# Performance work log

Measured on AMD Instinct MI355X. Metric: run time of the kernel, lower is better.

The kernel has to match this reference:

```python
import jax, jax.numpy as jnp
import numpy as np

HIDDEN = 2048
HEADS = 16
HEAD_DIM = HIDDEN // HEADS          # 128
KV_RANK = HIDDEN // 8               # 256 (kv_compression_ratio = 8)
ATTN_DIM = HEADS * HEAD_DIM         # 2048
EPS = 1e-6


def setup_inputs() -> dict:
    key = jax.random.key(0)
    ks = jax.random.split(key, 6)
    B, L = 2, 2048
    x = jax.random.normal(ks[0], (B, L, HIDDEN), dtype=jnp.float32)
    # weights stored [in, out] (torch Linear applies x @ W.T; same math)
    s = lambda fan_in: 1.0 / np.sqrt(fan_in)
    Wq = jax.random.normal(ks[1], (HIDDEN, ATTN_DIM), dtype=jnp.float32) * s(HIDDEN)
    Wkv_down = jax.random.normal(ks[2], (HIDDEN, KV_RANK), dtype=jnp.float32) * s(HIDDEN)
    kv_norm_w = jnp.ones((KV_RANK,), dtype=jnp.float32)
    Wkv_up = jax.random.normal(ks[3], (KV_RANK, 2 * ATTN_DIM), dtype=jnp.float32) * s(KV_RANK)
    Wo = jax.random.normal(ks[4], (ATTN_DIM, HIDDEN), dtype=jnp.float32) * s(ATTN_DIM)
    return {"x": x, "Wq": Wq, "Wkv_down": Wkv_down, "kv_norm_w": kv_norm_w,
            "Wkv_up": Wkv_up, "Wo": Wo}


def rms_norm(x, w):
    ms = jnp.mean(x * x, axis=-1, keepdims=True)
    return w * (x * jax.lax.rsqrt(ms + EPS))


def reference(x, Wq, Wkv_down, kv_norm_w, Wkv_up, Wo):
    B, L, D = x.shape
    q = (x @ Wq).reshape(B, L, HEADS, HEAD_DIM)
    latent = rms_norm(x @ Wkv_down, kv_norm_w)            # [B, L, KV_RANK]
    kv = latent @ Wkv_up                                   # [B, L, 2*ATTN_DIM]
    k, v = jnp.split(kv, 2, axis=-1)
    k = k.reshape(B, L, HEADS, HEAD_DIM)
    v = v.reshape(B, L, HEADS, HEAD_DIM)
    scores = jnp.einsum('bxhd,byhd->bhxy', q, k) / np.sqrt(HEAD_DIM)
    causal = jnp.tril(jnp.ones((L, L), dtype=bool))
    scores = jnp.where(causal, scores, -jnp.inf)
    attn = jax.nn.softmax(scores, axis=-1)
    out = jnp.einsum('bhxy,byhd->bxhd', attn, v).reshape(B, L, ATTN_DIM)
    return out @ Wo
```

## Files before the change

kernel.cpp:

```cpp
#include <hip/hip_runtime.h>
#include <cstdint>
#include <cstddef>

typedef unsigned short u16;
typedef __bf16 bf16x8 __attribute__((ext_vector_type(8)));
typedef __bf16 bf16x2 __attribute__((ext_vector_type(2)));
typedef float f32x4 __attribute__((ext_vector_type(4)));

__device__ inline u16 f2bf(float f) {
  uint32_t u = __builtin_bit_cast(uint32_t, f);
  u += 0x7fffu + ((u >> 16) & 1u);
  return (u16)(u >> 16);
}

#if defined(__has_builtin)
#if __has_builtin(__builtin_amdgcn_cvt_pk_bf16_f32)
#define HAVE_PK_BF16 1
#endif
#endif

__device__ inline uint32_t pk2bf(float a, float b) {
#ifdef HAVE_PK_BF16
  bf16x2 v = __builtin_amdgcn_cvt_pk_bf16_f32(a, b);
  return __builtin_bit_cast(uint32_t, v);
#else
  return (uint32_t)f2bf(a) | ((uint32_t)f2bf(b) << 16);
#endif
}

__device__ inline f32x4 mfma16(bf16x8 a, bf16x8 b, f32x4 c) {
  return __builtin_amdgcn_mfma_f32_16x16x32_bf16(a, b, c, 0, 0, 0);
}

__device__ inline void gl_lds16(const u16* g, u16* l) {
  __builtin_amdgcn_global_load_lds(
      (const __attribute__((address_space(1))) uint32_t*)g,
      (__attribute__((address_space(3))) uint32_t*)l, 16, 0, 0);
}

__device__ void tcvt_dev(const float* __restrict__ in, u16* __restrict__ out,
                         int R, int C, int bx, int by, float (*t)[33], int tid) {
  int cb = bx * 32, rb = by * 32;
  int x = tid & 31, y = tid >> 5;
#pragma unroll
  for (int k = 0; k < 4; ++k)
    t[y + k * 8][x] = in[(size_t)(rb + y + k * 8) * C + cb + x];
  __syncthreads();
#pragma unroll
  for (int k = 0; k < 4; ++k)
    out[(size_t)(cb + y + k * 8) * R + rb + x] = f2bf(t[x][y + k * 8]);
}

__global__ __launch_bounds__(256) void k_prep(
    const float* __restrict__ x, const float* __restrict__ Wq,
    const float* __restrict__ Wkvd, const float* __restrict__ Wkvu,
    const float* __restrict__ Wo, u16* __restrict__ xbf,
    u16* __restrict__ WqkdT, u16* __restrict__ WkvuT, u16* __restrict__ WoT) {
  __shared__ float t[32][33];
  int bid = blockIdx.x, tid = threadIdx.x;
  if (bid < 8192) {
    int i = bid * 256 + tid;
    const float4 v = ((const float4*)x)[i];
    ushort4 o;
    o.x = f2bf(v.x); o.y = f2bf(v.y); o.z = f2bf(v.z); o.w = f2bf(v.w);
    ((ushort4*)xbf)[i] = o;
  } else if (bid < 12288) {
    int q = bid - 8192;
    tcvt_dev(Wq, WqkdT, 2048, 2048, q & 63, q >> 6, t, tid);
  } else if (bid < 12800) {
    int q = bid - 12288;
    tcvt_dev(Wkvd, WqkdT + 2048 * 2048, 2048, 256, q & 7, q >> 3, t, tid);
  } else if (bid < 13824) {
    int q = bid - 12800;
    tcvt_dev(Wkvu, WkvuT, 256, 4096, q & 127, q >> 7, t, tid);
  } else {
    int q = bid - 13824;
    tcvt_dev(Wo, WoT, 2048, 2048, q & 63, q >> 6, t, tid);
  }
}

__global__ __launch_bounds__(256) void k_rmsn(const u16* __restrict__ qc,
                                              const float* __restrict__ w,
                                              u16* __restrict__ out) {
  int row = blockIdx.x * 4 + (threadIdx.x >> 6);
  int lane = threadIdx.x & 63;
  const ushort4 u = *(const ushort4*)(qc + (size_t)row * 2304 + 2048 + lane * 4);
  float4 v;
  v.x = __builtin_bit_cast(float, (uint32_t)u.x << 16);
  v.y = __builtin_bit_cast(float, (uint32_t)u.y << 16);
  v.z = __builtin_bit_cast(float, (uint32_t)u.z << 16);
  v.w = __builtin_bit_cast(float, (uint32_t)u.w << 16);
  float ss = v.x * v.x + v.y * v.y + v.z * v.z + v.w * v.w;
#pragma unroll
  for (int off = 1; off < 64; off <<= 1) ss += __shfl_xor(ss, off);
  float r = rsqrtf(ss * (1.f / 256.f) + 1e-6f);
  const float4 wv = ((const float4*)w)[lane];
  ushort4 o;
  o.x = f2bf(v.x * r * wv.x);
  o.y = f2bf(v.y * r * wv.y);
  o.z = f2bf(v.z * r * wv.z);
  o.w = f2bf(v.w * r * wv.w);
  *(ushort4*)(out + (size_t)row * 256 + lane * 4) = o;
}

template <int BK, int MODE>
__global__ __launch_bounds__(256) void k_gemm(const u16* __restrict__ A,
                                              const u16* __restrict__ BT,
                                              void* __restrict__ C,
                                              u16* __restrict__ C2, int K,
                                              int ldc, float scale) {
  __shared__ __align__(16) u16 As[128 * BK];
  __shared__ __align__(16) u16 Bs[128 * BK];
  const int tid = threadIdx.x, wave = tid >> 6, lane = tid & 63;
  const int lanem = lane & 15, quad = lane >> 4;
  const int m0 = blockIdx.x * 128, n0 = blockIdx.y * 128;
  const int wr = wave >> 1, wc = wave & 1;
  f32x4 acc[4][4] = {};
  for (int k0 = 0; k0 < K; k0 += BK) {
    __syncthreads();
    if constexpr (BK == 32) {
      const int srow = lane >> 2, scol = (lane & 3) * 8;
#pragma unroll
      for (int c = 0; c < 2; ++c) {
        int p = wave * 2 + c;
        gl_lds16(A + (size_t)(m0 + p * 16 + srow) * K + k0 + scol, &As[p * 512]);
        gl_lds16(BT + (size_t)(n0 + p * 16 + srow) * K + k0 + scol, &Bs[p * 512]);
      }
    } else {
      const int srow = lane >> 3;
      const int scol = ((lane & 7) ^ srow) * 8;
#pragma unroll
      for (int c = 0; c < 4; ++c) {
        int p = wave * 4 + c;
        gl_lds16(A + (size_t)(m0 + p * 8 + srow) * K + k0 + scol, &As[p * 512]);
        gl_lds16(BT + (size_t)(n0 + p * 8 + srow) * K + k0 + scol, &Bs[p * 512]);
      }
    }
    __syncthreads();
#pragma unroll
    for (int kk = 0; kk < BK / 32; ++kk) {
      bf16x8 af[4], bff[4];
      if constexpr (BK == 32) {
#pragma unroll
        for (int i = 0; i < 4; ++i)
          af[i] = *(const bf16x8*)&As[(wr * 64 + i * 16 + lanem) * 32 + quad * 8];
#pragma unroll
        for (int j = 0; j < 4; ++j)
          bff[j] = *(const bf16x8*)&Bs[(wc * 64 + j * 16 + lanem) * 32 + quad * 8];
      } else {
        const int kp = ((kk * 4 + quad) ^ (lanem & 7)) << 3;
#pragma unroll
        for (int i = 0; i < 4; ++i)
          af[i] = *(const bf16x8*)&As[(wr * 64 + i * 16 + lanem) * 64 + kp];
#pragma unroll
        for (int j = 0; j < 4; ++j)
          bff[j] = *(const bf16x8*)&Bs[(wc * 64 + j * 16 + lanem) * 64 + kp];
      }
#pragma unroll
      for (int i = 0; i < 4; ++i)
#pragma unroll
        for (int j = 0; j < 4; ++j)
          acc[i][j] = mfma16(af[i], bff[j], acc[i][j]);
    }
  }
#pragma unroll
  for (int i = 0; i < 4; ++i)
#pragma unroll
    for (int j = 0; j < 4; ++j)
#pragma unroll
      for (int r = 0; r < 4; ++r) {
        int row = m0 + wr * 64 + i * 16 + quad * 4 + r;
        int col = n0 + wc * 64 + j * 16 + lanem;
        float v = acc[i][j][r] * scale;
        if constexpr (MODE == 0) {
          ((float*)C)[(size_t)row * ldc + col] = v;
        } else if constexpr (MODE == 1) {
          ((u16*)C)[(size_t)row * ldc + col] = f2bf(v);
        } else {
          if (n0 < 2048) {
            ((u16*)C)[(size_t)row * 2048 + col] = f2bf(v);
          } else {
            int cc = col - 2048, hh = cc >> 7, dd = cc & 127;
            int bb = row >> 11, ll = row & 2047;
            C2[((size_t)(bb * 16 + hh) * 128 + dd) * 2048 + ll] = f2bf(v);
          }
        }
      }
}

__global__ __launch_bounds__(256) void k_attn(const u16* __restrict__ qg,
                                              const u16* __restrict__ kg,
                                              const u16* __restrict__ vtg,
                                              u16* __restrict__ ao) {
  __shared__ __align__(16) u16 Ks[2][64 * 128];
  __shared__ __align__(16) u16 VTs[2][128 * 64];
  __shared__ __align__(16) u16 Ps[4][16 * 72];
  const int bid = blockIdx.x;
  const int xcd = bid & 7, r5 = bid >> 3;
  const int bh = xcd * 4 + (r5 & 3), pairid = r5 >> 2;
  const int b = bh >> 4, h = bh & 15;
  const int tid = threadIdx.x, w = tid >> 6, lane = tid & 63;
  const int lanem = lane & 15, quad = lane >> 4;

  const int kr = lane >> 4, kc = lane & 15;
  const u16* kbp[4];
#pragma unroll
  for (int j = 0; j < 4; ++j) {
    int row = w * 16 + j * 4 + kr;
    kbp[j] = kg + (size_t)(b * 2048 + row) * 2048 + h * 128 +
             ((kc ^ (row & 15)) << 3);
  }
  const int vr = lane >> 3, vc = lane & 7;
  const u16* vbp[4];
#pragma unroll
  for (int j = 0; j < 4; ++j) {
    int row = w * 32 + j * 8 + vr;
    vbp[j] = vtg + (size_t)(bh * 128 + row) * 2048 + ((vc ^ vr) << 3);
  }

  const int qt0 = pairid, qt1 = 31 - pairid;
  int qb = qt0 * 64, nt = qt0 + 1, t = 0, qi = 0;

  bf16x8 qf[4];
  {
    const u16* qp = qg + (size_t)(b * 2048 + qb + w * 16 + lanem) * 2304 +
                    h * 128 + quad * 8;
#pragma unroll
    for (int c = 0; c < 4; ++c) qf[c] = *(const bf16x8*)(qp + c * 32);
  }
  f32x4 o[8] = {};
  float m_i = -1e30f, l_i = 0.f;

#pragma unroll
  for (int j = 0; j < 4; ++j) gl_lds16(kbp[j], &Ks[0][(w * 16 + j * 4) * 128]);
#pragma unroll
  for (int j = 0; j < 4; ++j) gl_lds16(vbp[j], &VTs[0][(w * 32 + j * 8) * 64]);

  for (int it = 0; it < 33; ++it) {
    __syncthreads();
    if (it + 1 < 33) {
      int t2 = (t + 1 == nt) ? 0 : t + 1;
      int nb = (it + 1) & 1;
      size_t ko = (size_t)t2 * (64 * 2048);
      int vo = t2 * 64;
#pragma unroll
      for (int j = 0; j < 4; ++j)
        gl_lds16(kbp[j] + ko, &Ks[nb][(w * 16 + j * 4) * 128]);
#pragma unroll
      for (int j = 0; j < 4; ++j)
        gl_lds16(vbp[j] + vo, &VTs[nb][(w * 32 + j * 8) * 64]);
    }
    const int buf = it & 1;
    f32x4 s[4] = {};
#pragma unroll
    for (int c = 0; c < 4; ++c) {
      const int kp = ((c * 4 + quad) ^ lanem) << 3;
#pragma unroll
      for (int ss = 0; ss < 4; ++ss) {
        bf16x8 kf = *(const bf16x8*)&Ks[buf][(ss * 16 + lanem) * 128 + kp];
        s[ss] = mfma16(kf, qf[c], s[ss]);
      }
    }
    if (t == nt - 1) {
      const int qq = w * 16 + lanem;
#pragma unroll
      for (int ss = 0; ss < 4; ++ss)
#pragma unroll
        for (int r = 0; r < 4; ++r)
          if (ss * 16 + quad * 4 + r > qq) s[ss][r] = -1e30f;
    }
    float mx = fmaxf(fmaxf(fmaxf(s[0][0], s[0][1]), fmaxf(s[0][2], s[0][3])),
                     fmaxf(fmaxf(s[1][0], s[1][1]), fmaxf(s[1][2], s[1][3])));
    mx = fmaxf(mx, fmaxf(fmaxf(fmaxf(s[2][0], s[2][1]), fmaxf(s[2][2], s[2][3])),
                         fmaxf(fmaxf(s[3][0], s[3][1]), fmaxf(s[3][2], s[3][3]))));
    mx = fmaxf(mx, __shfl_xor(mx, 16));
    mx = fmaxf(mx, __shfl_xor(mx, 32));
    const float mn = fmaxf(m_i, mx);
    float rs = 0.f;
#pragma unroll
    for (int ss = 0; ss < 4; ++ss)
#pragma unroll
      for (int r = 0; r < 4; ++r) {
        s[ss][r] = exp2f(s[ss][r] - mn);
        rs += s[ss][r];
      }
    rs += __shfl_xor(rs, 16);
    rs += __shfl_xor(rs, 32);
    if (__any(mx > m_i)) {
      const float al = exp2f(m_i - mn);
      l_i = l_i * al + rs;
      m_i = mn;
      float alr[4];
#pragma unroll
      for (int r = 0; r < 4; ++r)
        alr[r] = __shfl(al, (lane & 48) | (quad * 4 + r));
#pragma unroll
      for (int dc = 0; dc < 8; ++dc)
#pragma unroll
        for (int r = 0; r < 4; ++r) o[dc][r] *= alr[r];
    } else {
      l_i += rs;
    }
#pragma unroll
    for (int ss = 0; ss < 4; ++ss) {
      uint2 pp;
      pp.x = pk2bf(s[ss][0], s[ss][1]);
      pp.y = pk2bf(s[ss][2], s[ss][3]);
      *(uint2*)&Ps[w][lanem * 72 + ss * 16 + quad * 4] = pp;
    }
    bf16x8 pf0 = *(const bf16x8*)&Ps[w][lanem * 72 + quad * 8];
    bf16x8 pf1 = *(const bf16x8*)&Ps[w][lanem * 72 + 32 + quad * 8];
#pragma unroll
    for (int dc = 0; dc < 8; ++dc) {
      const int vrow = (dc * 16 + lanem) * 64;
      bf16x8 vf0 = *(const bf16x8*)&VTs[buf][vrow + ((quad ^ (lanem & 7)) << 3)];
      bf16x8 vf1 =
          *(const bf16x8*)&VTs[buf][vrow + (((4 + quad) ^ (lanem & 7)) << 3)];
      o[dc] = mfma16(pf0, vf0, o[dc]);
      o[dc] = mfma16(pf1, vf1, o[dc]);
    }
    if (++t == nt) {
      const float inv = 1.f / l_i;
      float invr[4];
#pragma unroll
      for (int r = 0; r < 4; ++r)
        invr[r] = __shfl(inv, (lane & 48) | (quad * 4 + r));
#pragma unroll
      for (int r = 0; r < 4; ++r) {
        u16* op = ao + (size_t)(b * 2048 + qb + w * 16 + quad * 4 + r) * 2048 +
                  h * 128;
#pragma unroll
        for (int dc = 0; dc < 8; ++dc)
          op[dc * 16 + lanem] = f2bf(o[dc][r] * invr[r]);
      }
      if (qi == 0) {
        qi = 1;
        qb = qt1 * 64;
        nt = qt1 + 1;
        t = 0;
        const u16* qp = qg + (size_t)(b * 2048 + qb + w * 16 + lanem) * 2304 +
                        h * 128 + quad * 8;
#pragma unroll
        for (int c = 0; c < 4; ++c) qf[c] = *(const bf16x8*)(qp + c * 32);
#pragma unroll
        for (int dc = 0; dc < 8; ++dc) o[dc] = f32x4{0.f, 0.f, 0.f, 0.f};
        m_i = -1e30f;
        l_i = 0.f;
      }
    }
  }
}

extern "C" void kernel_launch(void* const* d_in, const int* in_sizes, int n_in,
                              void* d_out, int out_size, void* d_ws, size_t ws_size,
                              hipStream_t stream) {
  const float* x    = (const float*)d_in[0];
  const float* Wq   = (const float*)d_in[1];
  const float* Wkvd = (const float*)d_in[2];
  const float* wn   = (const float*)d_in[3];
  const float* Wkvu = (const float*)d_in[4];
  const float* Wo   = (const float*)d_in[5];
  float* out = (float*)d_out;

  char* w0 = (char*)d_ws;
  u16* xbf   = (u16*)(w0);
  u16* qc    = (u16*)(w0 + 16777216);
  u16* WqkdT = (u16*)(w0 + 35651584);
  u16* WoT   = (u16*)(w0 + 45088768);
  u16* WkvuT = (u16*)(w0 + 53477376);
  u16* kbf   = (u16*)(w0 + 55574528);
  u16* vtbf  = (u16*)(w0 + 72351744);
  u16* latbf = WqkdT;
  u16* aobf  = xbf;

  const float sc2 = 0.08838834764831845f * 1.4426950408889634f;

  k_prep<<<17920, 256, 0, stream>>>(x, Wq, Wkvd, Wkvu, Wo, xbf, WqkdT, WkvuT, WoT);
  k_gemm<32, 1><<<dim3(32, 18), 256, 0, stream>>>(xbf, WqkdT, qc, nullptr, 2048,
                                                  2304, sc2);
  k_rmsn<<<1024, 256, 0, stream>>>(qc, wn, latbf);
  k_gemm<64, 2><<<dim3(32, 32), 256, 0, stream>>>(latbf, WkvuT, kbf, vtbf, 256,
                                                  0, 1.0f);
  k_attn<<<512, 256, 0, stream>>>(qc, kbf, vtbf, aobf);
  k_gemm<32, 0><<<dim3(32, 16), 256, 0, stream>>>(aobf, WoT, out, nullptr, 2048,
                                                  2048, 1.0f);
}
```

Measured before the change: 340.5 us.

## Transpose QK^T layout, compute softmax row sum via ones-column MFMA

The QK^T MFMA operands are swapped so each lane holds four query rows, and row max reductions now use DPP moves instead of cross-lane shuffles. The softmax denominator is computed by appending a block of ones to the V^T tile in LDS and running a ninth MFMA column block, which removes the scalar row-sum and the shuffle-based rescale broadcasts. The P tile in LDS is stored with an XOR swizzle and no padding. Separately, the KV-up GEMM epilogue writes transposed V as packed 4-element stores instead of scalar stores. In exchange it adds extra MFMAs, per-element bf16 stores into P, and more LDS for V^T.

```diff
diff --git a/kernel.cpp b/kernel.cpp
--- a/kernel.cpp
+++ b/kernel.cpp
@@ -13,21 +13,6 @@
   return (u16)(u >> 16);
 }
 
-#if defined(__has_builtin)
-#if __has_builtin(__builtin_amdgcn_cvt_pk_bf16_f32)
-#define HAVE_PK_BF16 1
-#endif
-#endif
-
-__device__ inline uint32_t pk2bf(float a, float b) {
-#ifdef HAVE_PK_BF16
-  bf16x2 v = __builtin_amdgcn_cvt_pk_bf16_f32(a, b);
-  return __builtin_bit_cast(uint32_t, v);
-#else
-  return (uint32_t)f2bf(a) | ((uint32_t)f2bf(b) << 16);
-#endif
-}
-
 __device__ inline f32x4 mfma16(bf16x8 a, bf16x8 b, f32x4 c) {
   return __builtin_amdgcn_mfma_f32_16x16x32_bf16(a, b, c, 0, 0, 0);
 }
@@ -36,6 +21,13 @@
   __builtin_amdgcn_global_load_lds(
       (const __attribute__((address_space(1))) uint32_t*)g,
       (__attribute__((address_space(3))) uint32_t*)l, 16, 0, 0);
+}
+
+template <int CTRL>
+__device__ inline float dppmax(float x) {
+  int y = __builtin_amdgcn_mov_dpp(__builtin_bit_cast(int, x), CTRL, 0xf, 0xf,
+                                   true);
+  return fmaxf(x, __builtin_bit_cast(float, y));
 }
 
 __device__ void tcvt_dev(const float* __restrict__ in, u16* __restrict__ out,
@@ -166,26 +158,33 @@
 #pragma unroll
   for (int i = 0; i < 4; ++i)
 #pragma unroll
-    for (int j = 0; j < 4; ++j)
+    for (int j = 0; j < 4; ++j) {
+      const int row0 = m0 + wr * 64 + i * 16 + quad * 4;
+      const int col = n0 + wc * 64 + j * 16 + lanem;
+      if constexpr (MODE == 2) {
+        if (col >= 2048) {
+          int cc = col - 2048, hh = cc >> 7, dd = cc & 127;
+          int bb = row0 >> 11, ll = row0 & 2047;
+          ushort4 pk;
+          pk.x = f2bf(acc[i][j][0]);
+          pk.y = f2bf(acc[i][j][1]);
+          pk.z = f2bf(acc[i][j][2]);
+          pk.w = f2bf(acc[i][j][3]);
+          *(ushort4*)&C2[((size_t)(bb * 16 + hh) * 128 + dd) * 2048 + ll] = pk;
+          continue;
+        }
+      }
 #pragma unroll
       for (int r = 0; r < 4; ++r) {
-        int row = m0 + wr * 64 + i * 16 + quad * 4 + r;
-        int col = n0 + wc * 64 + j * 16 + lanem;
         float v = acc[i][j][r] * scale;
-        if constexpr (MODE == 0) {
-          ((float*)C)[(size_t)row * ldc + col] = v;
-        } else if constexpr (MODE == 1) {
-          ((u16*)C)[(size_t)row * ldc + col] = f2bf(v);
-        } else {
-          if (n0 < 2048) {
-            ((u16*)C)[(size_t)row * 2048 + col] = f2bf(v);
-          } else {
-            int cc = col - 2048, hh = cc >> 7, dd = cc & 127;
-            int bb = row >> 11, ll = row & 2047;
-            C2[((size_t)(bb * 16 + hh) * 128 + dd) * 2048 + ll] = f2bf(v);
-          }
-        }
-      }
+        if constexpr (MODE == 0)
+          ((float*)C)[(size_t)(row0 + r) * ldc + col] = v;
+        else if constexpr (MODE == 1)
+          ((u16*)C)[(size_t)(row0 + r) * ldc + col] = f2bf(v);
+        else
+          ((u16*)C)[(size_t)(row0 + r) * 2048 + col] = f2bf(v);
+      }
+    }
 }
 
 __global__ __launch_bounds__(256) void k_attn(const u16* __restrict__ qg,
@@ -193,8 +192,8 @@
                                               const u16* __restrict__ vtg,
                                               u16* __restrict__ ao) {
   __shared__ __align__(16) u16 Ks[2][64 * 128];
-  __shared__ __align__(16) u16 VTs[2][128 * 64];
-  __shared__ __align__(16) u16 Ps[4][16 * 72];
+  __shared__ __align__(16) u16 VTs[2][144 * 64];
+  __shared__ __align__(16) u16 Ps[4][16 * 64];
   const int bid = blockIdx.x;
   const int xcd = bid & 7, r5 = bid >> 3;
   const int bh = xcd * 4 + (r5 & 3), pairid = r5 >> 2;
@@ -228,13 +227,20 @@
 #pragma unroll
     for (int c = 0; c < 4; ++c) qf[c] = *(const bf16x8*)(qp + c * 32);
   }
-  f32x4 o[8] = {};
-  float m_i = -1e30f, l_i = 0.f;
+  f32x4 o[9] = {};
+  float m_i[4] = {-1e30f, -1e30f, -1e30f, -1e30f};
 
 #pragma unroll
   for (int j = 0; j < 4; ++j) gl_lds16(kbp[j], &Ks[0][(w * 16 + j * 4) * 128]);
 #pragma unroll
   for (int j = 0; j < 4; ++j) gl_lds16(vbp[j], &VTs[0][(w * 32 + j * 8) * 64]);
+  {
+    const ushort4 ones4{0x3f80u, 0x3f80u, 0x3f80u, 0x3f80u};
+    for (int i = tid; i < 512; i += 256) {
+      int bufi = i >> 8, off = (i & 255) * 4;
+      *(ushort4*)&VTs[bufi][128 * 64 + off] = ones4;
+    }
+  }
 
   for (int it = 0; it < 33; ++it) {
     __syncthreads();
@@ -258,60 +264,53 @@
 #pragma unroll
       for (int ss = 0; ss < 4; ++ss) {
         bf16x8 kf = *(const bf16x8*)&Ks[buf][(ss * 16 + lanem) * 128 + kp];
-        s[ss] = mfma16(kf, qf[c], s[ss]);
+        s[ss] = mfma16(qf[c], kf, s[ss]);
       }
     }
     if (t == nt - 1) {
-      const int qq = w * 16 + lanem;
 #pragma unroll
       for (int ss = 0; ss < 4; ++ss)
 #pragma unroll
         for (int r = 0; r < 4; ++r)
-          if (ss * 16 + quad * 4 + r > qq) s[ss][r] = -1e30f;
-    }
-    float mx = fmaxf(fmaxf(fmaxf(s[0][0], s[0][1]), fmaxf(s[0][2], s[0][3])),
-                     fmaxf(fmaxf(s[1][0], s[1][1]), fmaxf(s[1][2], s[1][3])));
-    mx = fmaxf(mx, fmaxf(fmaxf(fmaxf(s[2][0], s[2][1]), fmaxf(s[2][2], s[2][3])),
-                         fmaxf(fmaxf(s[3][0], s[3][1]), fmaxf(s[3][2], s[3][3]))));
-    mx = fmaxf(mx, __shfl_xor(mx, 16));
-    mx = fmaxf(mx, __shfl_xor(mx, 32));
-    const float mn = fmaxf(m_i, mx);
-    float rs = 0.f;
-#pragma unroll
-    for (int ss = 0; ss < 4; ++ss)
+          if (ss * 16 + lanem > w * 16 + quad * 4 + r) s[ss][r] = -1e30f;
+    }
+    float mx[4], mn[4];
+#pragma unroll
+    for (int r = 0; r < 4; ++r) {
+      float m = fmaxf(fmaxf(s[0][r], s[1][r]), fmaxf(s[2][r], s[3][r]));
+      m = dppmax<0xB1>(m);
+      m = dppmax<0x4E>(m);
+      m = dppmax<0x141>(m);
+      m = dppmax<0x140>(m);
+      mx[r] = m;
+      mn[r] = fmaxf(m_i[r], m);
+    }
+    bool moved = (mx[0] > m_i[0]) | (mx[1] > m_i[1]) | (mx[2] > m_i[2]) |
+                 (mx[3] > m_i[3]);
+    if (__any(moved)) {
 #pragma unroll
       for (int r = 0; r < 4; ++r) {
-        s[ss][r] = exp2f(s[ss][r] - mn);
-        rs += s[ss][r];
-      }
-    rs += __shfl_xor(rs, 16);
-    rs += __shfl_xor(rs, 32);
-    if (__any(mx > m_i)) {
-      const float al = exp2f(m_i - mn);
-      l_i = l_i * al + rs;
-      m_i = mn;
-      float alr[4];
-#pragma unroll
-      for (int r = 0; r < 4; ++r)
-        alr[r] = __shfl(al, (lane & 48) | (quad * 4 + r));
-#pragma unroll
-      for (int dc = 0; dc < 8; ++dc)
-#pragma unroll
-        for (int r = 0; r < 4; ++r) o[dc][r] *= alr[r];
-    } else {
-      l_i += rs;
+        float al = exp2f(m_i[r] - mn[r]);
+        m_i[r] = mn[r];
+#pragma unroll
+        for (int dc = 0; dc < 9; ++dc) o[dc][r] *= al;
+      }
     }
 #pragma unroll
     for (int ss = 0; ss < 4; ++ss) {
-      uint2 pp;
-      pp.x = pk2bf(s[ss][0], s[ss][1]);
-      pp.y = pk2bf(s[ss][2], s[ss][3]);
-      *(uint2*)&Ps[w][lanem * 72 + ss * 16 + quad * 4] = pp;
-    }
-    bf16x8 pf0 = *(const bf16x8*)&Ps[w][lanem * 72 + quad * 8];
-    bf16x8 pf1 = *(const bf16x8*)&Ps[w][lanem * 72 + 32 + quad * 8];
-#pragma unroll
-    for (int dc = 0; dc < 8; ++dc) {
+      const int g = ss * 2 + (lanem >> 3);
+#pragma unroll
+      for (int r = 0; r < 4; ++r) {
+        const int row = quad * 4 + r;
+        Ps[w][row * 64 + ((g ^ (row & 7)) << 3) + (lanem & 7)] =
+            f2bf(exp2f(s[ss][r] - mn[r]));
+      }
+    }
+    bf16x8 pf0 = *(const bf16x8*)&Ps[w][lanem * 64 + ((quad ^ (lanem & 7)) << 3)];
+    bf16x8 pf1 =
+        *(const bf16x8*)&Ps[w][lanem * 64 + (((4 + quad) ^ (lanem & 7)) << 3)];
+#pragma unroll
+    for (int dc = 0; dc < 9; ++dc) {
       const int vrow = (dc * 16 + lanem) * 64;
       bf16x8 vf0 = *(const bf16x8*)&VTs[buf][vrow + ((quad ^ (lanem & 7)) << 3)];
       bf16x8 vf1 =
@@ -320,18 +319,14 @@
       o[dc] = mfma16(pf1, vf1, o[dc]);
     }
     if (++t == nt) {
-      const float inv = 1.f / l_i;
-      float invr[4];
-#pragma unroll
-      for (int r = 0; r < 4; ++r)
-        invr[r] = __shfl(inv, (lane & 48) | (quad * 4 + r));
 #pragma unroll
       for (int r = 0; r < 4; ++r) {
+        const float inv = 1.f / o[8][r];
         u16* op = ao + (size_t)(b * 2048 + qb + w * 16 + quad * 4 + r) * 2048 +
                   h * 128;
 #pragma unroll
         for (int dc = 0; dc < 8; ++dc)
-          op[dc * 16 + lanem] = f2bf(o[dc][r] * invr[r]);
+          op[dc * 16 + lanem] = f2bf(o[dc][r] * inv);
       }
       if (qi == 0) {
         qi = 1;
@@ -343,9 +338,9 @@
 #pragma unroll
         for (int c = 0; c < 4; ++c) qf[c] = *(const bf16x8*)(qp + c * 32);
 #pragma unroll
-        for (int dc = 0; dc < 8; ++dc) o[dc] = f32x4{0.f, 0.f, 0.f, 0.f};
-        m_i = -1e30f;
-        l_i = 0.f;
+        for (int dc = 0; dc < 9; ++dc) o[dc] = f32x4{0.f, 0.f, 0.f, 0.f};
+#pragma unroll
+        for (int r = 0; r < 4; ++r) m_i[r] = -1e30f;
       }
     }
   }
```

New measurement: 332.2 us. 2.4% less time.
